# Kernel optimization log

Hardware: AMD Instinct MI355X
Metric: run time of the kernel (lower is better)

Reference implementation:

```python
import jax, jax.numpy as jnp
import numpy as np

# dims
C = 256; G = 16; GC = C // G; K = 3; P = K * K
N, H, W = 8, 56, 56
HID = int(C * 4.0)
PAD = 1; STRIDE = 1; DIL = 1
OFFSET_SCALE = 1.0
LN_EPS = 1e-6


def setup_inputs() -> dict:
    key = jax.random.key(0)
    ks = jax.random.split(key, 16)
    rn = lambda k, shape, s: jax.random.normal(k, shape, jnp.float32) * s
    return {
        "x": rn(ks[0], (N, H, W, C), 1.0),
        "norm1_g": jnp.ones((C,), jnp.float32), "norm1_b": jnp.zeros((C,), jnp.float32),
        "norm2_g": jnp.ones((C,), jnp.float32), "norm2_b": jnp.zeros((C,), jnp.float32),
        "gamma1": jnp.ones((C,), jnp.float32), "gamma2": jnp.ones((C,), jnp.float32),
        "dw_w": rn(ks[1], (C, 1, K, K), 0.1), "dw_b": rn(ks[2], (C,), 0.02),
        "dwln_g": jnp.ones((C,), jnp.float32), "dwln_b": jnp.zeros((C,), jnp.float32),
        "off_w": rn(ks[3], (C, G * P * 2), 0.01), "off_b": rn(ks[4], (G * P * 2,), 0.01),
        "mask_w": rn(ks[5], (C, G * P), 0.02), "mask_b": rn(ks[6], (G * P,), 0.02),
        "in_w": rn(ks[7], (C, C), C ** -0.5), "in_b": jnp.zeros((C,), jnp.float32),
        "out_w": rn(ks[8], (C, C), C ** -0.5), "out_b": jnp.zeros((C,), jnp.float32),
        "fc1_w": rn(ks[9], (C, HID), C ** -0.5), "fc1_b": jnp.zeros((HID,), jnp.float32),
        "fc2_w": rn(ks[10], (HID, C), HID ** -0.5), "fc2_b": jnp.zeros((C,), jnp.float32),
    }


def layer_norm(x, g, b):
    mu = x.mean(-1, keepdims=True)
    var = ((x - mu) ** 2).mean(-1, keepdims=True)
    return (x - mu) * jax.lax.rsqrt(var + LN_EPS) * g + b


def depthwise_conv(x, w, b):
    # x: (N,H,W,C), w: (C,1,K,K) depthwise
    y = jax.lax.conv_general_dilated(
        x.transpose(0, 3, 1, 2), w, (1, 1), ((PAD, PAD), (PAD, PAD)),
        feature_group_count=C)
    return y.transpose(0, 2, 3, 1) + b


def bilinear_gather(img, gx, gy):
    # img: (Hp,Wp,GC); gx,gy: (L,) normalized grid coords in [-1,1]
    # F.grid_sample(mode='bilinear', padding_mode='zeros', align_corners=False)
    Hp, Wp = img.shape[0], img.shape[1]
    x = (gx + 1.0) * 0.5 * Wp - 0.5
    y = (gy + 1.0) * 0.5 * Hp - 0.5
    x0 = jnp.floor(x); y0 = jnp.floor(y)
    lx = x - x0; ly = y - y0

    def tap(yi, xi, wgt):
        valid = (yi >= 0) & (yi < Hp) & (xi >= 0) & (xi < Wp)
        yc = jnp.clip(yi, 0, Hp - 1).astype(jnp.int32)
        xc = jnp.clip(xi, 0, Wp - 1).astype(jnp.int32)
        return jnp.where(valid, wgt, 0.0)[:, None] * img[yc, xc]  # (L,GC)

    return (tap(y0, x0, (1 - lx) * (1 - ly)) + tap(y0, x0 + 1, lx * (1 - ly))
            + tap(y0 + 1, x0, (1 - lx) * ly) + tap(y0 + 1, x0 + 1, lx * ly))


def dcnv3(xin, dw_w, dw_b, dwln_g, dwln_b, off_w, off_b, mask_w, mask_b,
          in_w, in_b, out_w, out_b):
    # xin: (N,H,W,C)
    xproj = xin @ in_w + in_b
    x1 = depthwise_conv(xin, dw_w, dw_b)
    x1 = jax.nn.gelu(layer_norm(x1, dwln_g, dwln_b), approximate=False)
    offset = x1 @ off_w + off_b                                   # (N,H,W,G*P*2)
    mask = jax.nn.softmax((x1 @ mask_w + mask_b).reshape(N, H, W, G, P), axis=-1)

    xp = jnp.pad(xproj, ((0, 0), (PAD, PAD), (PAD, PAD), (0, 0)))
    Hp, Wp = H + 2 * PAD, W + 2 * PAD

    # reference points, normalized by padded spatial shape; last dim = (x,y)
    base = (DIL * (K - 1)) // 2 + 0.5
    ref_y = (base + jnp.arange(H, dtype=jnp.float32) * STRIDE) / Hp
    ref_x = (base + jnp.arange(W, dtype=jnp.float32) * STRIDE) / Wp
    ref = jnp.stack(jnp.broadcast_arrays(ref_x[None, :], ref_y[:, None]), -1)  # (H,W,2)

    # dilation grid, x-major flatten order (torch meshgrid 'ij' on (x,y))
    lin = -float((DIL * (K - 1)) // 2) + jnp.arange(K, dtype=jnp.float32) * DIL
    gx, gy = jnp.meshgrid(lin, lin, indexing='ij')  # gx varies along dim0
    gridpts = jnp.stack([gx / Wp, gy / Hp], -1).reshape(P, 2)

    off = offset.reshape(N, H, W, G, P, 2) * OFFSET_SCALE / jnp.array([Wp, Hp], jnp.float32)
    loc = (ref[None, :, :, None, None, :] + gridpts[None, None, None, None, :, :] * OFFSET_SCALE
           + off)                                                 # (N,H,W,G,P,2)
    sg = 2.0 * loc - 1.0

    # per-group images and sampling grids
    img = xp.reshape(N, Hp, Wp, G, GC).transpose(0, 3, 1, 2, 4).reshape(N * G, Hp, Wp, GC)
    gxs = sg[..., 0].transpose(0, 3, 1, 2, 4).reshape(N * G, H * W * P)
    gys = sg[..., 1].transpose(0, 3, 1, 2, 4).reshape(N * G, H * W * P)
    sampled = jax.vmap(bilinear_gather)(img, gxs, gys)            # (N*G, H*W*P, GC)
    sampled = sampled.reshape(N, G, H, W, P, GC)

    out = jnp.einsum('nghwpc,nhwgp->nhwgc', sampled, mask).reshape(N, H, W, C)
    return out @ out_w + out_b


def reference(x, norm1_g, norm1_b, norm2_g, norm2_b, gamma1, gamma2,
              dw_w, dw_b, dwln_g, dwln_b, off_w, off_b, mask_w, mask_b,
              in_w, in_b, out_w, out_b, fc1_w, fc1_b, fc2_w, fc2_b):
    h = dcnv3(layer_norm(x, norm1_g, norm1_b), dw_w, dw_b, dwln_g, dwln_b,
              off_w, off_b, mask_w, mask_b, in_w, in_b, out_w, out_b)
    x = x + gamma1 * h
    m = jax.nn.gelu(layer_norm(x, norm2_g, norm2_b) @ fc1_w + fc1_b,
                    approximate=False) @ fc2_w + fc2_b
    return x + gamma2 * m
```

## Files before the change

### kernel.cpp

```cpp
#include <hip/hip_runtime.h>
#include <math.h>

#define NB 8
#define HH 56
#define WWD 56
#define CC 256
#define PIX (NB*HH*WWD)

typedef __attribute__((ext_vector_type(8))) short bf16x8;
typedef __attribute__((ext_vector_type(4))) float f32x4;

__device__ __forceinline__ float gelu_exact(float v) {
    return 0.5f * v * (1.0f + erff(v * 0.70710678118654752f));
}
__device__ __forceinline__ unsigned short f2bf(float f) {
    unsigned u = __float_as_uint(f);
    unsigned r = (u + 0x7fffu + ((u >> 16) & 1u)) >> 16;
    return (unsigned short)r;
}
__device__ __forceinline__ float bf2f(unsigned short b) {
    return __uint_as_float(((unsigned)b) << 16);
}
__device__ __forceinline__ void gl_lds16(const void* g, void* l) {
    __builtin_amdgcn_global_load_lds(
        (const __attribute__((address_space(1))) void*)g,
        (__attribute__((address_space(3))) void*)l, 16, 0, 0);
}
__device__ __forceinline__ void wave_reduce2(float& s, float& sq) {
    #pragma unroll
    for (int o = 32; o >= 1; o >>= 1) {
        s  += __shfl_xor(s, o);
        sq += __shfl_xor(sq, o);
    }
}

__global__ __launch_bounds__(256) void prep_kernel(
    const float* __restrict__ inw, const float* __restrict__ offw,
    const float* __restrict__ offb, const float* __restrict__ mskw,
    const float* __restrict__ mskb, const float* __restrict__ outw,
    const float* __restrict__ f1w, const float* __restrict__ f2w,
    const float* __restrict__ dww,
    unsigned short* __restrict__ bt_in, unsigned short* __restrict__ bt_om,
    unsigned short* __restrict__ bt_out, unsigned short* __restrict__ bt_fc1,
    unsigned short* __restrict__ bt_fc2, float* __restrict__ wt9,
    float* __restrict__ bias_om)
{
    int i = blockIdx.x * 256 + threadIdx.x;
    if (i < 65536) {
        int n = i >> 8, k = i & 255;
        bt_in[i] = f2bf(inw[(size_t)k*256 + n]);
    } else if (i < 196608) {
        int j = i - 65536;
        int n = j >> 8, k = j & 255;
        float v = (n < 288) ? offw[(size_t)k*288 + n]
                : (n < 432) ? mskw[(size_t)k*144 + (n-288)] : 0.f;
        bt_om[j] = f2bf(v);
    } else if (i < 262144) {
        int j = i - 196608;
        int n = j >> 8, k = j & 255;
        bt_out[j] = f2bf(outw[(size_t)k*256 + n]);
    } else if (i < 524288) {
        int j = i - 262144;
        int n = j >> 8, k = j & 255;
        bt_fc1[j] = f2bf(f1w[(size_t)k*1024 + n]);
    } else if (i < 786432) {
        int j = i - 524288;
        int n = j >> 10, k = j & 1023;
        bt_fc2[j] = f2bf(f2w[(size_t)k*256 + n]);
    } else if (i < 788736) {
        int j = i - 786432;
        int t = j >> 8, c = j & 255;
        wt9[j] = dww[(size_t)c*9 + t];
    } else if (i < 789248) {
        int j = i - 788736;
        bias_om[j] = (j < 288) ? offb[j] : (j < 432) ? mskb[j-288] : 0.f;
    }
}

__global__ __launch_bounds__(256) void ln_bf_kernel(
    const float* __restrict__ in, const float* __restrict__ g,
    const float* __restrict__ b, unsigned short* __restrict__ out)
{
    int wave = threadIdx.x >> 6, lane = threadIdx.x & 63;
    int pix = blockIdx.x * 4 + wave;
    int c0 = lane * 4;
    float4 v = *reinterpret_cast<const float4*>(&in[(size_t)pix * CC + c0]);
    float s = v.x + v.y + v.z + v.w;
    float sq = v.x*v.x + v.y*v.y + v.z*v.z + v.w*v.w;
    wave_reduce2(s, sq);
    float mu = s * (1.0f/256.0f);
    float var = sq * (1.0f/256.0f) - mu*mu;
    float rs = rsqrtf(var + 1e-6f);
    float4 gv = *reinterpret_cast<const float4*>(&g[c0]);
    float4 bv = *reinterpret_cast<const float4*>(&b[c0]);
    ushort4 o;
    o.x = f2bf((v.x-mu)*rs*gv.x + bv.x);
    o.y = f2bf((v.y-mu)*rs*gv.y + bv.y);
    o.z = f2bf((v.z-mu)*rs*gv.z + bv.z);
    o.w = f2bf((v.w-mu)*rs*gv.w + bv.w);
    *reinterpret_cast<ushort4*>(&out[(size_t)pix * CC + c0]) = o;
}

__global__ __launch_bounds__(256) void dwconv_ln_gelu_kernel(
    const unsigned short* __restrict__ xl, const float* __restrict__ wt9,
    const float* __restrict__ cb, const float* __restrict__ lg,
    const float* __restrict__ lb, unsigned short* __restrict__ out)
{
    int bid = blockIdx.x;
    int wg = (bid & 7) * (gridDim.x >> 3) + (bid >> 3);
    int wave = threadIdx.x >> 6, lane = threadIdx.x & 63;
    int pix0 = wg * 16 + wave * 4;
    int n = pix0 / (HH*WWD); int rem = pix0 % (HH*WWD);
    int h = rem / WWD, wb = rem % WWD;
    int c0 = lane * 4;

    float4 wv[9];
    #pragma unroll
    for (int t = 0; t < 9; ++t)
        wv[t] = *reinterpret_cast<const float4*>(&wt9[t*256 + c0]);
    float4 cbv = *reinterpret_cast<const float4*>(&cb[c0]);
    float4 gv  = *reinterpret_cast<const float4*>(&lg[c0]);
    float4 bv  = *reinterpret_cast<const float4*>(&lb[c0]);

    float4 a[4];
    #pragma unroll
    for (int px = 0; px < 4; ++px) a[px] = cbv;

    #pragma unroll
    for (int r = 0; r < 3; ++r) {
        int hh = h + r - 1;
        if (hh < 0 || hh >= HH) continue;
        const unsigned short* rowp = xl + (((size_t)n*HH + hh)*WWD)*CC + c0;
        #pragma unroll
        for (int dc = 0; dc < 6; ++dc) {
            int cc = wb - 1 + dc;
            if (cc < 0 || cc >= WWD) continue;
            ushort4 xv = *reinterpret_cast<const ushort4*>(&rowp[(size_t)cc*CC]);
            float fx = bf2f(xv.x), fy = bf2f(xv.y), fz = bf2f(xv.z), fw = bf2f(xv.w);
            #pragma unroll
            for (int px = 0; px < 4; ++px) {
                int kx = dc - px;
                if (kx >= 0 && kx < 3) {
                    float4 wq = wv[r*3 + kx];
                    a[px].x += fx*wq.x; a[px].y += fy*wq.y;
                    a[px].z += fz*wq.z; a[px].w += fw*wq.w;
                }
            }
        }
    }

    #pragma unroll
    for (int px = 0; px < 4; ++px) {
        float s = a[px].x + a[px].y + a[px].z + a[px].w;
        float sq = a[px].x*a[px].x + a[px].y*a[px].y + a[px].z*a[px].z + a[px].w*a[px].w;
        wave_reduce2(s, sq);
        float mu = s*(1.f/256.f), var = sq*(1.f/256.f) - mu*mu;
        float rs = rsqrtf(var + 1e-6f);
        ushort4 o;
        o.x = f2bf(gelu_exact((a[px].x-mu)*rs*gv.x + bv.x));
        o.y = f2bf(gelu_exact((a[px].y-mu)*rs*gv.y + bv.y));
        o.z = f2bf(gelu_exact((a[px].z-mu)*rs*gv.z + bv.z));
        o.w = f2bf(gelu_exact((a[px].w-mu)*rs*gv.w + bv.w));
        *reinterpret_cast<ushort4*>(&out[(size_t)(pix0+px)*CC + c0]) = o;
    }
}

template<int EPI>
__global__ __launch_bounds__(256, 4) void gemm_v4(
    const unsigned short* __restrict__ A, const unsigned short* __restrict__ Bt,
    const float* __restrict__ bias, float* __restrict__ Cf, float* __restrict__ Cf2,
    unsigned short* __restrict__ Cb, int M, int N, int K,
    const float* __restrict__ extra1, const float* __restrict__ extra2,
    const float* __restrict__ lng, const float* __restrict__ lnb)
{
    __shared__ unsigned short Al[16384];
    __shared__ float S1[4][64], S2[4][64];
    const int tid = threadIdx.x;
    const int wave = tid >> 6, lane = tid & 63;
    const int lm = lane & 15, kq = lane >> 4;

    int bid = blockIdx.x + blockIdx.y * gridDim.x;
    int nwg = gridDim.x * gridDim.y;
    int wg = (bid & 7) * (nwg >> 3) + (bid >> 3);
    const int m0 = (wg / gridDim.x) * 64;
    const int n0 = (wg % gridDim.x) * 256;
    const int n0w = n0 + wave * 64;

    f32x4 acc[4][4];
    #pragma unroll
    for (int i = 0; i < 4; ++i)
        #pragma unroll
        for (int j = 0; j < 4; ++j)
            acc[i][j] = (f32x4){0.f, 0.f, 0.f, 0.f};

    const unsigned short* Bw = Bt + (size_t)(n0w + lm) * K;

    const int nch = K >> 8;
    for (int ch = 0; ch < nch; ++ch) {
        if (ch) __syncthreads();
        int kc = ch << 8;
        #pragma unroll
        for (int jr = 0; jr < 8; ++jr) {
            int idx = jr*256 + tid;
            int kb = idx >> 6, row = idx & 63;
            gl_lds16(A + (size_t)(m0+row)*K + kc + kb*8,
                     (char*)Al + (jr*4 + wave)*1024);
        }
        __syncthreads();
        #pragma unroll
        for (int ks = 0; ks < 8; ++ks) {
            int kb = ks*4 + kq;
            bf16x8 af[4], bf[4];
            #pragma unroll
            for (int mi = 0; mi < 4; ++mi)
                af[mi] = *reinterpret_cast<const bf16x8*>(
                    &Al[(kb*64 + mi*16 + lm)*8]);
            #pragma unroll
            for (int ni = 0; ni < 4; ++ni)
                bf[ni] = *reinterpret_cast<const bf16x8*>(
                    &Bw[(size_t)ni*16*K + kc + ks*32 + kq*8]);
            #pragma unroll
            for (int mi = 0; mi < 4; ++mi)
                #pragma unroll
                for (int ni = 0; ni < 4; ++ni)
                    acc[mi][ni] = __builtin_amdgcn_mfma_f32_16x16x32_bf16(
                        af[mi], bf[ni], acc[mi][ni], 0, 0, 0);
        }
    }

    if (EPI == 5) {
        #pragma unroll
        for (int mi = 0; mi < 4; ++mi) {
            #pragma unroll
            for (int j = 0; j < 4; ++j) {
                int r = m0 + mi*16 + kq*4 + j;
                float ps = 0.f, pq = 0.f;
                #pragma unroll
                for (int ni = 0; ni < 4; ++ni) {
                    int c = n0w + ni*16 + lm;
                    float v = acc[mi][ni][j] + bias[c];
                    float xr = extra1[(size_t)r*N + c] + extra2[c]*v;
                    acc[mi][ni][j] = xr;
                    ps += xr; pq += xr*xr;
                }
                #pragma unroll
                for (int o = 8; o >= 1; o >>= 1) {
                    ps += __shfl_xor(ps, o);
                    pq += __shfl_xor(pq, o);
                }
                if (lm == 0) {
                    S1[wave][mi*16 + kq*4 + j] = ps;
                    S2[wave][mi*16 + kq*4 + j] = pq;
                }
            }
        }
        __syncthreads();
        #pragma unroll
        for (int mi = 0; mi < 4; ++mi) {
            #pragma unroll
            for (int j = 0; j < 4; ++j) {
                int rl = mi*16 + kq*4 + j;
                int r = m0 + rl;
                float s = S1[0][rl] + S1[1][rl] + S1[2][rl] + S1[3][rl];
                float sq = S2[0][rl] + S2[1][rl] + S2[2][rl] + S2[3][rl];
                float mu = s*(1.f/256.f), var = sq*(1.f/256.f) - mu*mu;
                float rs = rsqrtf(var + 1e-6f);
                #pragma unroll
                for (int ni = 0; ni < 4; ++ni) {
                    int c = n0w + ni*16 + lm;
                    float xr = acc[mi][ni][j];
                    Cf[(size_t)r*N + c] = xr;
                    Cb[(size_t)r*N + c] = f2bf((xr-mu)*rs*lng[c] + lnb[c]);
                }
            }
        }
        return;
    }

    #pragma unroll
    for (int mi = 0; mi < 4; ++mi) {
        #pragma unroll
        for (int ni = 0; ni < 4; ++ni) {
            int c = n0w + ni*16 + lm;
            float bb = bias[c];
            #pragma unroll
            for (int j = 0; j < 4; ++j) {
                int r = m0 + mi*16 + kq*4 + j;
                float v = acc[mi][ni][j] + bb;
                if (EPI == 1) {
                    Cb[(size_t)r*N + c] = f2bf(gelu_exact(v));
                } else if (EPI == 2) {
                    size_t gi = (size_t)r*N + c;
                    Cf[gi] = extra1[gi] + extra2[c]*v;
                } else if (EPI == 3) {
                    Cb[(size_t)r*N + c] = f2bf(v);
                } else if (EPI == 4) {
                    if (c < 288)      Cf [(size_t)r*288 + c]       = v;
                    else if (c < 432) Cf2[(size_t)r*144 + (c-288)] = v;
                }
            }
        }
    }
}

__device__ __forceinline__ void tap4b(const unsigned short* __restrict__ img, int yi, int xi,
                                      float wgt, float4& s) {
    if (yi >= 1 && yi <= 56 && xi >= 1 && xi <= 56) {
        ushort4 v = *reinterpret_cast<const ushort4*>(
            &img[(((size_t)(yi-1))*WWD + (xi-1)) * CC]);
        s.x += wgt*bf2f(v.x); s.y += wgt*bf2f(v.y);
        s.z += wgt*bf2f(v.z); s.w += wgt*bf2f(v.w);
    }
}

__global__ __launch_bounds__(256) void dcn_sample_kernel(
    const unsigned short* __restrict__ xproj, const float* __restrict__ offs,
    const float* __restrict__ msk, unsigned short* __restrict__ dcn)
{
    int bid = blockIdx.x;
    int wg = (bid & 7) * (gridDim.x >> 3) + (bid >> 3);
    int wave = threadIdx.x >> 6, lane = threadIdx.x & 63;
    int pix = wg * 4 + wave;
    int n = pix / (HH*WWD); int rem = pix % (HH*WWD);
    int h = rem / WWD, w = rem % WWD;
    int g = lane >> 2, c4 = lane & 3;
    const float* op = offs + (size_t)pix*288 + g*18;
    const float* mp = msk + (size_t)pix*144 + g*9;
    const unsigned short* img = xproj + (size_t)n*(HH*WWD*CC) + g*16 + c4*4;

    float mv[9]; float mx = -1e30f;
    #pragma unroll
    for (int j = 0; j < 9; ++j) { mv[j] = mp[j]; mx = fmaxf(mx, mv[j]); }
    float ssum = 0.f;
    #pragma unroll
    for (int j = 0; j < 9; ++j) { mv[j] = expf(mv[j]-mx); ssum += mv[j]; }
    float minv = 1.f/ssum;

    float4 acc = {0.f, 0.f, 0.f, 0.f};
    #pragma unroll
    for (int p = 0; p < 9; ++p) {
        float ox = op[p*2+0], oy = op[p*2+1];
        float xs = (float)(w + p/3) + ox;
        float ys = (float)(h + p%3) + oy;
        float x0f = floorf(xs), y0f = floorf(ys);
        float lx = xs - x0f, ly = ys - y0f;
        int x0 = (int)x0f, y0 = (int)y0f;
        float4 s = {0.f, 0.f, 0.f, 0.f};
        tap4b(img, y0,   x0,   (1.f-lx)*(1.f-ly), s);
        tap4b(img, y0,   x0+1, lx*(1.f-ly),       s);
        tap4b(img, y0+1, x0,   (1.f-lx)*ly,       s);
        tap4b(img, y0+1, x0+1, lx*ly,             s);
        float m = mv[p]*minv;
        acc.x += m*s.x; acc.y += m*s.y; acc.z += m*s.z; acc.w += m*s.w;
    }
    ushort4 o;
    o.x = f2bf(acc.x); o.y = f2bf(acc.y); o.z = f2bf(acc.z); o.w = f2bf(acc.w);
    *reinterpret_cast<ushort4*>(&dcn[(size_t)pix*CC + g*16 + c4*4]) = o;
}

extern "C" void kernel_launch(void* const* d_in, const int* in_sizes, int n_in,
                              void* d_out, int out_size, void* d_ws, size_t ws_size,
                              hipStream_t stream)
{
    const float* x    = (const float*)d_in[0];
    const float* n1g  = (const float*)d_in[1];
    const float* n1b  = (const float*)d_in[2];
    const float* n2g  = (const float*)d_in[3];
    const float* n2b  = (const float*)d_in[4];
    const float* g1   = (const float*)d_in[5];
    const float* g2   = (const float*)d_in[6];
    const float* dww  = (const float*)d_in[7];
    const float* dwb  = (const float*)d_in[8];
    const float* dlng = (const float*)d_in[9];
    const float* dlnb = (const float*)d_in[10];
    const float* offw = (const float*)d_in[11];
    const float* offb = (const float*)d_in[12];
    const float* mskw = (const float*)d_in[13];
    const float* mskb = (const float*)d_in[14];
    const float* inw  = (const float*)d_in[15];
    const float* inb  = (const float*)d_in[16];
    const float* outw = (const float*)d_in[17];
    const float* outb = (const float*)d_in[18];
    const float* f1w  = (const float*)d_in[19];
    const float* f1b  = (const float*)d_in[20];
    const float* f2w  = (const float*)d_in[21];
    const float* f2b  = (const float*)d_in[22];
    float* out = (float*)d_out;

    char* base = (char*)d_ws;
    unsigned short* xl_bf    = (unsigned short*)(base + 0);
    unsigned short* xproj_bf = (unsigned short*)(base + 12845056);
    float*          xres     = (float*)(base + 25690112);
    unsigned short* x1_bf    = (unsigned short*)(base + 51380224);
    float*          offs     = (float*)(base + 64225280);
    float*          msk      = (float*)(base + 93126656);
    unsigned short* dcn_bf   = xl_bf;
    unsigned short* y2_bf    = x1_bf;
    unsigned short* h1       = (unsigned short*)(base + 64225280);
    unsigned short* btb      = (unsigned short*)(base + 115605504);
    unsigned short* bt_in  = btb + 0;
    unsigned short* bt_om  = btb + 65536;
    unsigned short* bt_out = btb + 196608;
    unsigned short* bt_fc1 = btb + 262144;
    unsigned short* bt_fc2 = btb + 524288;
    float*          wt9     = (float*)(btb + 786432);
    float*          bias_om = (float*)(btb + 805888);

    prep_kernel<<<3084, 256, 0, stream>>>(inw, offw, offb, mskw, mskb, outw,
        f1w, f2w, dww, bt_in, bt_om, bt_out, bt_fc1, bt_fc2, wt9, bias_om);

    ln_bf_kernel<<<PIX/4, 256, 0, stream>>>(x, n1g, n1b, xl_bf);
    gemm_v4<3><<<dim3(1,392), 256, 0, stream>>>(xl_bf, bt_in, inb, nullptr, nullptr,
        xproj_bf, PIX, 256, 256, nullptr, nullptr, nullptr, nullptr);
    dwconv_ln_gelu_kernel<<<PIX/16, 256, 0, stream>>>(xl_bf, wt9, dwb, dlng, dlnb, x1_bf);
    gemm_v4<4><<<dim3(2,392), 256, 0, stream>>>(x1_bf, bt_om, bias_om, offs, msk,
        nullptr, PIX, 512, 256, nullptr, nullptr, nullptr, nullptr);
    dcn_sample_kernel<<<PIX/4, 256, 0, stream>>>(xproj_bf, offs, msk, dcn_bf);
    gemm_v4<5><<<dim3(1,392), 256, 0, stream>>>(dcn_bf, bt_out, outb, xres, nullptr,
        y2_bf, PIX, 256, 256, x, g1, n2g, n2b);
    gemm_v4<1><<<dim3(4,392), 256, 0, stream>>>(y2_bf, bt_fc1, f1b, nullptr, nullptr,
        h1, PIX, 1024, 256, nullptr, nullptr, nullptr, nullptr);
    gemm_v4<2><<<dim3(1,392), 256, 0, stream>>>(h1, bt_fc2, f2b, out, nullptr,
        nullptr, PIX, 256, 1024, xres, g2, nullptr, nullptr);
}
```

Measured before the change: 254.3 us.

## Fuse MLP fc1/GELU/fc2 into one kernel and store offsets/masks in bf16

Adds an mlp_kernel that computes fc1, applies GELU, and feeds 256-column hidden chunks through LDS straight into the fc2 accumulation. This removes the global round trip of the large 1024-wide hidden activation and one launch. The offset/mask GEMM output is also switched from fp32 to bf16, halving that write and the read in the sampler, at some precision cost on the sampling coordinates. The fused kernel uses smaller 32-row tiles and reads B weights directly from global memory without LDS staging, which may reduce MFMA efficiency.

```diff
diff --git a/kernel.cpp b/kernel.cpp
--- a/kernel.cpp
+++ b/kernel.cpp
@@ -6,6 +6,7 @@
 #define WWD 56
 #define CC 256
 #define PIX (NB*HH*WWD)
+#define HPAD 264
 
 typedef __attribute__((ext_vector_type(8))) short bf16x8;
 typedef __attribute__((ext_vector_type(4))) float f32x4;
@@ -287,17 +288,128 @@
             for (int j = 0; j < 4; ++j) {
                 int r = m0 + mi*16 + kq*4 + j;
                 float v = acc[mi][ni][j] + bb;
-                if (EPI == 1) {
-                    Cb[(size_t)r*N + c] = f2bf(gelu_exact(v));
-                } else if (EPI == 2) {
-                    size_t gi = (size_t)r*N + c;
-                    Cf[gi] = extra1[gi] + extra2[c]*v;
-                } else if (EPI == 3) {
+                if (EPI == 3) {
                     Cb[(size_t)r*N + c] = f2bf(v);
                 } else if (EPI == 4) {
-                    if (c < 288)      Cf [(size_t)r*288 + c]       = v;
-                    else if (c < 432) Cf2[(size_t)r*144 + (c-288)] = v;
-                }
+                    if (c < 288)
+                        ((unsigned short*)Cf)[(size_t)r*288 + c] = f2bf(v);
+                    else if (c < 432)
+                        ((unsigned short*)Cf2)[(size_t)r*144 + (c-288)] = f2bf(v);
+                }
+            }
+        }
+    }
+}
+
+__global__ __launch_bounds__(256, 3) void mlp_kernel(
+    const unsigned short* __restrict__ A,
+    const unsigned short* __restrict__ B1,
+    const float* __restrict__ b1,
+    const unsigned short* __restrict__ B2,
+    const float* __restrict__ b2,
+    const float* __restrict__ xres, const float* __restrict__ g2,
+    float* __restrict__ out)
+{
+    __shared__ unsigned short Alds[8192];
+    __shared__ unsigned short Hlds[32*HPAD];
+    const int tid = threadIdx.x;
+    const int wave = tid >> 6, lane = tid & 63;
+    const int lm = lane & 15, kq = lane >> 4;
+
+    int bid = blockIdx.x;
+    int nwg = gridDim.x;
+    int wg = (bid & 7) * (nwg >> 3) + (bid >> 3);
+    const int m0 = wg * 32;
+
+    #pragma unroll
+    for (int jr = 0; jr < 4; ++jr) {
+        int idx = jr*256 + tid;
+        int kb = idx >> 5, row = idx & 31;
+        gl_lds16(A + (size_t)(m0+row)*256 + kb*8, (char*)Alds + (jr*4 + wave)*1024);
+    }
+    __syncthreads();
+
+    f32x4 acc2[2][4];
+    #pragma unroll
+    for (int i = 0; i < 2; ++i)
+        #pragma unroll
+        for (int j = 0; j < 4; ++j)
+            acc2[i][j] = (f32x4){0.f, 0.f, 0.f, 0.f};
+
+    for (int ch = 0; ch < 4; ++ch) {
+        f32x4 acc1[2][4];
+        #pragma unroll
+        for (int i = 0; i < 2; ++i)
+            #pragma unroll
+            for (int j = 0; j < 4; ++j)
+                acc1[i][j] = (f32x4){0.f, 0.f, 0.f, 0.f};
+
+        const unsigned short* Bw1 = B1 + (size_t)(ch*256 + wave*64 + lm)*256;
+        #pragma unroll
+        for (int ks = 0; ks < 8; ++ks) {
+            bf16x8 af[2], bf[4];
+            #pragma unroll
+            for (int mi = 0; mi < 2; ++mi)
+                af[mi] = *reinterpret_cast<const bf16x8*>(
+                    &Alds[((ks*4+kq)*32 + mi*16 + lm)*8]);
+            #pragma unroll
+            for (int ni = 0; ni < 4; ++ni)
+                bf[ni] = *reinterpret_cast<const bf16x8*>(
+                    &Bw1[(size_t)ni*16*256 + ks*32 + kq*8]);
+            #pragma unroll
+            for (int mi = 0; mi < 2; ++mi)
+                #pragma unroll
+                for (int ni = 0; ni < 4; ++ni)
+                    acc1[mi][ni] = __builtin_amdgcn_mfma_f32_16x16x32_bf16(
+                        af[mi], bf[ni], acc1[mi][ni], 0, 0, 0);
+        }
+        #pragma unroll
+        for (int mi = 0; mi < 2; ++mi) {
+            #pragma unroll
+            for (int ni = 0; ni < 4; ++ni) {
+                int cl = wave*64 + ni*16 + lm;
+                float bb = b1[ch*256 + cl];
+                #pragma unroll
+                for (int j = 0; j < 4; ++j) {
+                    int r = mi*16 + kq*4 + j;
+                    Hlds[r*HPAD + cl] = f2bf(gelu_exact(acc1[mi][ni][j] + bb));
+                }
+            }
+        }
+        __syncthreads();
+        const unsigned short* Bw2 = B2 + (size_t)(wave*64 + lm)*1024 + ch*256;
+        #pragma unroll
+        for (int ks = 0; ks < 8; ++ks) {
+            bf16x8 af[2], bf[4];
+            #pragma unroll
+            for (int mi = 0; mi < 2; ++mi)
+                af[mi] = *reinterpret_cast<const bf16x8*>(
+                    &Hlds[(mi*16 + lm)*HPAD + ks*32 + kq*8]);
+            #pragma unroll
+            for (int ni = 0; ni < 4; ++ni)
+                bf[ni] = *reinterpret_cast<const bf16x8*>(
+                    &Bw2[(size_t)ni*16*1024 + ks*32 + kq*8]);
+            #pragma unroll
+            for (int mi = 0; mi < 2; ++mi)
+                #pragma unroll
+                for (int ni = 0; ni < 4; ++ni)
+                    acc2[mi][ni] = __builtin_amdgcn_mfma_f32_16x16x32_bf16(
+                        af[mi], bf[ni], acc2[mi][ni], 0, 0, 0);
+        }
+        __syncthreads();
+    }
+
+    #pragma unroll
+    for (int mi = 0; mi < 2; ++mi) {
+        #pragma unroll
+        for (int ni = 0; ni < 4; ++ni) {
+            int c = wave*64 + ni*16 + lm;
+            float bb = b2[c], gg = g2[c];
+            #pragma unroll
+            for (int j = 0; j < 4; ++j) {
+                int r = m0 + mi*16 + kq*4 + j;
+                size_t gi = (size_t)r*256 + c;
+                out[gi] = xres[gi] + gg*(acc2[mi][ni][j] + bb);
             }
         }
     }
@@ -314,8 +426,8 @@
 }
 
 __global__ __launch_bounds__(256) void dcn_sample_kernel(
-    const unsigned short* __restrict__ xproj, const float* __restrict__ offs,
-    const float* __restrict__ msk, unsigned short* __restrict__ dcn)
+    const unsigned short* __restrict__ xproj, const unsigned short* __restrict__ offs,
+    const unsigned short* __restrict__ msk, unsigned short* __restrict__ dcn)
 {
     int bid = blockIdx.x;
     int wg = (bid & 7) * (gridDim.x >> 3) + (bid >> 3);
@@ -324,13 +436,13 @@
     int n = pix / (HH*WWD); int rem = pix % (HH*WWD);
     int h = rem / WWD, w = rem % WWD;
     int g = lane >> 2, c4 = lane & 3;
-    const float* op = offs + (size_t)pix*288 + g*18;
-    const float* mp = msk + (size_t)pix*144 + g*9;
+    const unsigned short* op = offs + (size_t)pix*288 + g*18;
+    const unsigned short* mp = msk + (size_t)pix*144 + g*9;
     const unsigned short* img = xproj + (size_t)n*(HH*WWD*CC) + g*16 + c4*4;
 
     float mv[9]; float mx = -1e30f;
     #pragma unroll
-    for (int j = 0; j < 9; ++j) { mv[j] = mp[j]; mx = fmaxf(mx, mv[j]); }
+    for (int j = 0; j < 9; ++j) { mv[j] = bf2f(mp[j]); mx = fmaxf(mx, mv[j]); }
     float ssum = 0.f;
     #pragma unroll
     for (int j = 0; j < 9; ++j) { mv[j] = expf(mv[j]-mx); ssum += mv[j]; }
@@ -339,7 +451,7 @@
     float4 acc = {0.f, 0.f, 0.f, 0.f};
     #pragma unroll
     for (int p = 0; p < 9; ++p) {
-        float ox = op[p*2+0], oy = op[p*2+1];
+        float ox = bf2f(op[p*2+0]), oy = bf2f(op[p*2+1]);
         float xs = (float)(w + p/3) + ox;
         float ys = (float)(h + p%3) + oy;
         float x0f = floorf(xs), y0f = floorf(ys);
@@ -392,12 +504,11 @@
     unsigned short* xproj_bf = (unsigned short*)(base + 12845056);
     float*          xres     = (float*)(base + 25690112);
     unsigned short* x1_bf    = (unsigned short*)(base + 51380224);
-    float*          offs     = (float*)(base + 64225280);
-    float*          msk      = (float*)(base + 93126656);
+    unsigned short* offs_bf  = (unsigned short*)(base + 64225280);
+    unsigned short* msk_bf   = (unsigned short*)(base + 78675968);
     unsigned short* dcn_bf   = xl_bf;
     unsigned short* y2_bf    = x1_bf;
-    unsigned short* h1       = (unsigned short*)(base + 64225280);
-    unsigned short* btb      = (unsigned short*)(base + 115605504);
+    unsigned short* btb      = (unsigned short*)(base + 85901312);
     unsigned short* bt_in  = btb + 0;
     unsigned short* bt_om  = btb + 65536;
     unsigned short* bt_out = btb + 196608;
@@ -413,13 +524,12 @@
     gemm_v4<3><<<dim3(1,392), 256, 0, stream>>>(xl_bf, bt_in, inb, nullptr, nullptr,
         xproj_bf, PIX, 256, 256, nullptr, nullptr, nullptr, nullptr);
     dwconv_ln_gelu_kernel<<<PIX/16, 256, 0, stream>>>(xl_bf, wt9, dwb, dlng, dlnb, x1_bf);
-    gemm_v4<4><<<dim3(2,392), 256, 0, stream>>>(x1_bf, bt_om, bias_om, offs, msk,
-        nullptr, PIX, 512, 256, nullptr, nullptr, nullptr, nullptr);
-    dcn_sample_kernel<<<PIX/4, 256, 0, stream>>>(xproj_bf, offs, msk, dcn_bf);
+    gemm_v4<4><<<dim3(2,392), 256, 0, stream>>>(x1_bf, bt_om, bias_om,
+        (float*)offs_bf, (float*)msk_bf, nullptr, PIX, 512, 256,
+        nullptr, nullptr, nullptr, nullptr);
+    dcn_sample_kernel<<<PIX/4, 256, 0, stream>>>(xproj_bf, offs_bf, msk_bf, dcn_bf);
     gemm_v4<5><<<dim3(1,392), 256, 0, stream>>>(dcn_bf, bt_out, outb, xres, nullptr,
         y2_bf, PIX, 256, 256, x, g1, n2g, n2b);
-    gemm_v4<1><<<dim3(4,392), 256, 0, stream>>>(y2_bf, bt_fc1, f1b, nullptr, nullptr,
-        h1, PIX, 1024, 256, nullptr, nullptr, nullptr, nullptr);
-    gemm_v4<2><<<dim3(1,392), 256, 0, stream>>>(h1, bt_fc2, f2b, out, nullptr,
-        nullptr, PIX, 256, 1024, xres, g2, nullptr, nullptr);
-}
+    mlp_kernel<<<PIX/32, 256, 0, stream>>>(y2_bf, bt_fc1, f1b, bt_fc2, f2b,
+        xres, g2, out);
+}
```

New measurement: 289.2 us. +13.7%, slower.

## Store offsets and mask in bf16 and widen DCN sampling to 8 channels

Applied to the files above, without the earlier changes.

The offset/mask GEMM epilogue now writes bf16 instead of fp32, which halves the write traffic of that GEMM and the read traffic of the sampling kernel. The sampling kernel now has each lane handle 8 channels with 16-byte loads, processing two pixels per wave, so the grid is halved. The cost is lower precision in the sampling offsets: bf16 keeps few fractional bits at coordinates near 56, which can move the bilinear weights and affect accuracy.

```diff
diff --git a/kernel.cpp b/kernel.cpp
--- a/kernel.cpp
+++ b/kernel.cpp
@@ -8,6 +8,7 @@
 #define PIX (NB*HH*WWD)
 
 typedef __attribute__((ext_vector_type(8))) short bf16x8;
+typedef __attribute__((ext_vector_type(8))) unsigned short u16x8;
 typedef __attribute__((ext_vector_type(4))) float f32x4;
 
 __device__ __forceinline__ float gelu_exact(float v) {
@@ -295,67 +296,71 @@
                 } else if (EPI == 3) {
                     Cb[(size_t)r*N + c] = f2bf(v);
                 } else if (EPI == 4) {
-                    if (c < 288)      Cf [(size_t)r*288 + c]       = v;
-                    else if (c < 432) Cf2[(size_t)r*144 + (c-288)] = v;
+                    if (c < 288)
+                        ((unsigned short*)Cf)[(size_t)r*288 + c] = f2bf(v);
+                    else if (c < 432)
+                        ((unsigned short*)Cf2)[(size_t)r*144 + (c-288)] = f2bf(v);
                 }
             }
         }
     }
 }
 
-__device__ __forceinline__ void tap4b(const unsigned short* __restrict__ img, int yi, int xi,
-                                      float wgt, float4& s) {
+__device__ __forceinline__ void tap8(const unsigned short* __restrict__ img, int yi, int xi,
+                                     float wgt, float* s) {
     if (yi >= 1 && yi <= 56 && xi >= 1 && xi <= 56) {
-        ushort4 v = *reinterpret_cast<const ushort4*>(
+        u16x8 v = *reinterpret_cast<const u16x8*>(
             &img[(((size_t)(yi-1))*WWD + (xi-1)) * CC]);
-        s.x += wgt*bf2f(v.x); s.y += wgt*bf2f(v.y);
-        s.z += wgt*bf2f(v.z); s.w += wgt*bf2f(v.w);
+        #pragma unroll
+        for (int k = 0; k < 8; ++k) s[k] += wgt*bf2f(v[k]);
     }
 }
 
 __global__ __launch_bounds__(256) void dcn_sample_kernel(
-    const unsigned short* __restrict__ xproj, const float* __restrict__ offs,
-    const float* __restrict__ msk, unsigned short* __restrict__ dcn)
+    const unsigned short* __restrict__ xproj, const unsigned short* __restrict__ offs,
+    const unsigned short* __restrict__ msk, unsigned short* __restrict__ dcn)
 {
     int bid = blockIdx.x;
     int wg = (bid & 7) * (gridDim.x >> 3) + (bid >> 3);
     int wave = threadIdx.x >> 6, lane = threadIdx.x & 63;
-    int pix = wg * 4 + wave;
+    int px = lane >> 5, g = (lane >> 1) & 15, c8 = lane & 1;
+    int pix = wg * 8 + wave * 2 + px;
     int n = pix / (HH*WWD); int rem = pix % (HH*WWD);
     int h = rem / WWD, w = rem % WWD;
-    int g = lane >> 2, c4 = lane & 3;
-    const float* op = offs + (size_t)pix*288 + g*18;
-    const float* mp = msk + (size_t)pix*144 + g*9;
-    const unsigned short* img = xproj + (size_t)n*(HH*WWD*CC) + g*16 + c4*4;
+    const unsigned short* op = offs + (size_t)pix*288 + g*18;
+    const unsigned short* mp = msk + (size_t)pix*144 + g*9;
+    const unsigned short* img = xproj + (size_t)n*(HH*WWD*CC) + g*16 + c8*8;
 
     float mv[9]; float mx = -1e30f;
     #pragma unroll
-    for (int j = 0; j < 9; ++j) { mv[j] = mp[j]; mx = fmaxf(mx, mv[j]); }
+    for (int j = 0; j < 9; ++j) { mv[j] = bf2f(mp[j]); mx = fmaxf(mx, mv[j]); }
     float ssum = 0.f;
     #pragma unroll
     for (int j = 0; j < 9; ++j) { mv[j] = expf(mv[j]-mx); ssum += mv[j]; }
     float minv = 1.f/ssum;
 
-    float4 acc = {0.f, 0.f, 0.f, 0.f};
+    float acc[8] = {0.f,0.f,0.f,0.f,0.f,0.f,0.f,0.f};
     #pragma unroll
     for (int p = 0; p < 9; ++p) {
-        float ox = op[p*2+0], oy = op[p*2+1];
+        float ox = bf2f(op[p*2+0]), oy = bf2f(op[p*2+1]);
         float xs = (float)(w + p/3) + ox;
         float ys = (float)(h + p%3) + oy;
         float x0f = floorf(xs), y0f = floorf(ys);
         float lx = xs - x0f, ly = ys - y0f;
         int x0 = (int)x0f, y0 = (int)y0f;
-        float4 s = {0.f, 0.f, 0.f, 0.f};
-        tap4b(img, y0,   x0,   (1.f-lx)*(1.f-ly), s);
-        tap4b(img, y0,   x0+1, lx*(1.f-ly),       s);
-        tap4b(img, y0+1, x0,   (1.f-lx)*ly,       s);
-        tap4b(img, y0+1, x0+1, lx*ly,             s);
+        float s[8] = {0.f,0.f,0.f,0.f,0.f,0.f,0.f,0.f};
+        tap8(img, y0,   x0,   (1.f-lx)*(1.f-ly), s);
+        tap8(img, y0,   x0+1, lx*(1.f-ly),       s);
+        tap8(img, y0+1, x0,   (1.f-lx)*ly,       s);
+        tap8(img, y0+1, x0+1, lx*ly,             s);
         float m = mv[p]*minv;
-        acc.x += m*s.x; acc.y += m*s.y; acc.z += m*s.z; acc.w += m*s.w;
-    }
-    ushort4 o;
-    o.x = f2bf(acc.x); o.y = f2bf(acc.y); o.z = f2bf(acc.z); o.w = f2bf(acc.w);
-    *reinterpret_cast<ushort4*>(&dcn[(size_t)pix*CC + g*16 + c4*4]) = o;
+        #pragma unroll
+        for (int k = 0; k < 8; ++k) acc[k] += m*s[k];
+    }
+    u16x8 o;
+    #pragma unroll
+    for (int k = 0; k < 8; ++k) o[k] = f2bf(acc[k]);
+    *reinterpret_cast<u16x8*>(&dcn[(size_t)pix*CC + g*16 + c8*8]) = o;
 }
 
 extern "C" void kernel_launch(void* const* d_in, const int* in_sizes, int n_in,
@@ -392,8 +397,8 @@
     unsigned short* xproj_bf = (unsigned short*)(base + 12845056);
     float*          xres     = (float*)(base + 25690112);
     unsigned short* x1_bf    = (unsigned short*)(base + 51380224);
-    float*          offs     = (float*)(base + 64225280);
-    float*          msk      = (float*)(base + 93126656);
+    unsigned short* offs_bf  = (unsigned short*)(base + 64225280);
+    unsigned short* msk_bf   = (unsigned short*)(base + 78675968);
     unsigned short* dcn_bf   = xl_bf;
     unsigned short* y2_bf    = x1_bf;
     unsigned short* h1       = (unsigned short*)(base + 64225280);
@@ -413,9 +418,10 @@
     gemm_v4<3><<<dim3(1,392), 256, 0, stream>>>(xl_bf, bt_in, inb, nullptr, nullptr,
         xproj_bf, PIX, 256, 256, nullptr, nullptr, nullptr, nullptr);
     dwconv_ln_gelu_kernel<<<PIX/16, 256, 0, stream>>>(xl_bf, wt9, dwb, dlng, dlnb, x1_bf);
-    gemm_v4<4><<<dim3(2,392), 256, 0, stream>>>(x1_bf, bt_om, bias_om, offs, msk,
-        nullptr, PIX, 512, 256, nullptr, nullptr, nullptr, nullptr);
-    dcn_sample_kernel<<<PIX/4, 256, 0, stream>>>(xproj_bf, offs, msk, dcn_bf);
+    gemm_v4<4><<<dim3(2,392), 256, 0, stream>>>(x1_bf, bt_om, bias_om,
+        (float*)offs_bf, (float*)msk_bf, nullptr, PIX, 512, 256,
+        nullptr, nullptr, nullptr, nullptr);
+    dcn_sample_kernel<<<PIX/8, 256, 0, stream>>>(xproj_bf, offs_bf, msk_bf, dcn_bf);
     gemm_v4<5><<<dim3(1,392), 256, 0, stream>>>(dcn_bf, bt_out, outb, xres, nullptr,
         y2_bf, PIX, 256, 256, x, g1, n2g, n2b);
     gemm_v4<1><<<dim3(4,392), 256, 0, stream>>>(y2_bf, bt_fc1, f1b, nullptr, nullptr,
```

New measurement: 244.2 us. -4.0%, faster.
